# Kernel optimization log

Measured on AMD Instinct MI355X. Metric: run time of the kernel, lower is better.

Reference implementation:

```python
import jax, jax.numpy as jnp
import numpy as np

HIDDEN = 256
HEADS = 8
HEAD_DIM = HIDDEN // HEADS
SCALE = HEAD_DIM ** -0.5


def setup_inputs() -> dict:
    key = jax.random.key(0)
    ks = jax.random.split(key, 12)
    B, N = 2, 2048
    s = lambda fan_in: 1.0 / np.sqrt(fan_in)
    inp = {
        'x': jax.random.normal(ks[0], (B, N, HIDDEN), jnp.float32),
        'coords': jax.random.normal(ks[1], (B, N, 3), jnp.float32),
        'W_qkv': jax.random.normal(ks[2], (HIDDEN, 3 * HIDDEN), jnp.float32) * s(HIDDEN),
        'W_out': jax.random.normal(ks[3], (HIDDEN, HIDDEN), jnp.float32) * s(HIDDEN),
        'b_out': jnp.zeros((HIDDEN,), jnp.float32),
        'pos_w1': jax.random.normal(ks[4], (3, 16), jnp.float32) * s(3),
        'pos_b1': jnp.zeros((16,), jnp.float32),
        'pos_w2': jax.random.normal(ks[5], (16, HEADS), jnp.float32) * s(16),
        'pos_b2': jnp.zeros((HEADS,), jnp.float32),
        'sym_w1': jax.random.normal(ks[6], (3, 16), jnp.float32) * s(3),
        'sym_b1': jnp.zeros((16,), jnp.float32),
        'sym_w2': jax.random.normal(ks[7], (16, HEADS), jnp.float32) * s(16),
        'sym_b2': jnp.zeros((HEADS,), jnp.float32),
    }
    return inp


def _bias_mlp(rel, w1, b1, w2, b2):
    # rel: [B,N,N,3] -> [B,H,N,N]
    h = jax.nn.relu(jnp.einsum('bijc,ck->bijk', rel, w1) + b1)
    out = jnp.einsum('bijk,kh->bijh', h, w2) + b2
    return jnp.transpose(out, (0, 3, 1, 2))


def reference(x, coords, W_qkv, W_out, b_out, pos_w1, pos_b1, pos_w2, pos_b2,
              sym_w1, sym_b1, sym_w2, sym_b2):
    B, N, C = x.shape
    qkv = (x @ W_qkv).reshape(B, N, 3, HEADS, HEAD_DIM)
    qkv = jnp.transpose(qkv, (2, 0, 3, 1, 4))  # [3,B,H,N,D]
    q, k, v = qkv[0], qkv[1], qkv[2]
    dots = jnp.einsum('bhid,bhjd->bhij', q, k) * SCALE
    rel_pos = coords[:, :, None, :] - coords[:, None, :, :]  # [B,N,N,3]
    reflect = jnp.array([-1.0, 1.0, 1.0], dtype=coords.dtype)
    coords_sym = coords * reflect
    sym_rel_pos = coords[:, :, None, :] - coords_sym[:, None, :, :]
    bias_direct = _bias_mlp(rel_pos, pos_w1, pos_b1, pos_w2, pos_b2)
    bias_sym = _bias_mlp(sym_rel_pos, sym_w1, sym_b1, sym_w2, sym_b2)
    attn = jax.nn.softmax(dots + bias_direct + bias_sym, axis=-1)
    out = jnp.einsum('bhij,bhjd->bhid', attn, v)
    out = jnp.transpose(out, (0, 2, 1, 3)).reshape(B, N, C)
    return out @ W_out + b_out
```

## Files before the change

### kernel.cpp

```cpp
#include <hip/hip_runtime.h>
#include <hip/hip_fp16.h>

typedef _Float16 half8_t __attribute__((ext_vector_type(8)));
typedef _Float16 half4_t __attribute__((ext_vector_type(4)));
typedef _Float16 h2      __attribute__((ext_vector_type(2)));
typedef float    f32x4   __attribute__((ext_vector_type(4)));

#define LOG2E 1.4426950408889634f
#define KSCALE (0.17677669529663687f * LOG2E)

#if __has_builtin(__builtin_amdgcn_exp2f)
#define EXP2F(x) __builtin_amdgcn_exp2f(x)
#else
#define EXP2F(x) exp2f(x)
#endif

template <int N>
__device__ __forceinline__ int dpp_ror(int v) {
  return __builtin_amdgcn_update_dpp(0, v, 0x120 + N, 0xf, 0xf, true);
}
__device__ __forceinline__ h2 rowmax16_h2(h2 v) {
  int t;
  t = dpp_ror<1>(__builtin_bit_cast(int, v));
  v = __builtin_elementwise_max(v, __builtin_bit_cast(h2, t));
  t = dpp_ror<2>(__builtin_bit_cast(int, v));
  v = __builtin_elementwise_max(v, __builtin_bit_cast(h2, t));
  t = dpp_ror<4>(__builtin_bit_cast(int, v));
  v = __builtin_elementwise_max(v, __builtin_bit_cast(h2, t));
  t = dpp_ror<8>(__builtin_bit_cast(int, v));
  v = __builtin_elementwise_max(v, __builtin_bit_cast(h2, t));
  return v;
}

__global__ __launch_bounds__(256) void prep_misc(
    const float* __restrict__ Wqkv, const float* __restrict__ Wout,
    const float* __restrict__ coords,
    const float* __restrict__ pw1, const float* __restrict__ pb1,
    const float* __restrict__ sw1, const float* __restrict__ sb1,
    _Float16* __restrict__ WqkvT, _Float16* __restrict__ WoutT,
    _Float16* __restrict__ APre, _Float16* __restrict__ BPre)
{
  __shared__ float tile[64][65];
  const int bi = blockIdx.x, tid = threadIdx.x;
  if (bi < 64) {
    const float* src; _Float16* dst; int t, W;
    if (bi < 48) { t = bi;      src = Wqkv; dst = WqkvT; W = 768; }
    else         { t = bi - 48; src = Wout; dst = WoutT; W = 256; }
    const int nOT = W >> 6;
    const int tk = t / nOT, to = t % nOT;
    const int cx = tid & 63, ry = tid >> 6;
#pragma unroll
    for (int rr = 0; rr < 16; ++rr) {
      const int kl = rr * 4 + ry;
      tile[kl][cx] = src[(tk * 64 + kl) * W + to * 64 + cx];
    }
    __syncthreads();
#pragma unroll
    for (int rr = 0; rr < 16; ++rr) {
      const int ol = rr * 4 + ry;
      dst[(to * 64 + ol) * 256 + tk * 64 + cx] = (_Float16)tile[cx][ol];
    }
  } else {
    const int row = (bi - 64) * 256 + tid;
    const float c0 = coords[row * 3 + 0];
    const float c1 = coords[row * 3 + 1];
    const float c2 = coords[row * 3 + 2];
#pragma unroll
    for (int k = 0; k < 16; ++k) {
      float a = c0 * pw1[k] + c1 * pw1[16 + k] + c2 * pw1[32 + k];
      APre[row * 32 + k] = (_Float16)(a + pb1[k]);
      BPre[row * 32 + k] = (_Float16)a;
      float s  =  c0 * sw1[k] + c1 * sw1[16 + k] + c2 * sw1[32 + k];
      float sb = -c0 * sw1[k] + c1 * sw1[16 + k] + c2 * sw1[32 + k];
      APre[row * 32 + 16 + k] = (_Float16)(s + sb1[k]);
      BPre[row * 32 + 16 + k] = (_Float16)sb;
    }
  }
}

__global__ __launch_bounds__(256) void qkv_gemm(
    const float* __restrict__ x, const _Float16* __restrict__ WqkvT,
    _Float16* __restrict__ Qh, _Float16* __restrict__ Kh,
    _Float16* __restrict__ Vt)
{
  __shared__ __align__(16) _Float16 tbuf[4][1536];
  const int wv = threadIdx.x >> 6;
  const int wg = blockIdx.x * 4 + wv;
  const int ti = wg / 12, og = wg % 12;
  const int i0 = ti * 16, o0 = og * 64;
  const int lane = threadIdx.x & 63, q = lane >> 4, c = lane & 15;
  f32x4 acc[4] = {{0,0,0,0},{0,0,0,0},{0,0,0,0},{0,0,0,0}};
  const float*    arow = x + (i0 + c) * 256;
  const _Float16* brow = WqkvT + (o0 + c) * 256;
#pragma unroll
  for (int k0 = 0; k0 < 256; k0 += 32) {
    f32x4 a0 = *reinterpret_cast<const f32x4*>(arow + k0 + q * 8);
    f32x4 a1 = *reinterpret_cast<const f32x4*>(arow + k0 + q * 8 + 4);
    half8_t af;
    af[0] = (_Float16)a0[0]; af[1] = (_Float16)a0[1];
    af[2] = (_Float16)a0[2]; af[3] = (_Float16)a0[3];
    af[4] = (_Float16)a1[0]; af[5] = (_Float16)a1[1];
    af[6] = (_Float16)a1[2]; af[7] = (_Float16)a1[3];
#pragma unroll
    for (int t = 0; t < 4; ++t) {
      half8_t bf = *reinterpret_cast<const half8_t*>(brow + t * 16 * 256 + k0 + q * 8);
      acc[t] = __builtin_amdgcn_mfma_f32_16x16x32_f16(af, bf, acc[t], 0, 0, 0);
    }
  }
  const int b = i0 >> 11, n0 = i0 & 2047;
  _Float16* vt = tbuf[wv];
  if (og < 8) {
#pragma unroll
    for (int t = 0; t < 4; ++t)
#pragma unroll
      for (int r = 0; r < 4; ++r)
        vt[(q * 4 + r) * 72 + t * 16 + c] = (_Float16)acc[t][r];
    asm volatile("s_waitcnt lgkmcnt(0)" ::: "memory");
    __builtin_amdgcn_sched_barrier(0);
    const int nl = lane & 15, seg = lane >> 4;
    const int o_g = o0 + seg * 16;
    const int h = (o_g >> 5) & 7, dbase = o_g & 31;
    _Float16* dst = ((o_g >> 8) == 0 ? Qh : Kh) +
                    ((b * 8 + h) * 2048 + n0 + nl) * 32 + dbase;
    half8_t r0 = *reinterpret_cast<const half8_t*>(vt + nl * 72 + seg * 16);
    half8_t r1 = *reinterpret_cast<const half8_t*>(vt + nl * 72 + seg * 16 + 8);
    *reinterpret_cast<half8_t*>(dst)     = r0;
    *reinterpret_cast<half8_t*>(dst + 8) = r1;
  } else {
#pragma unroll
    for (int t = 0; t < 4; ++t)
#pragma unroll
      for (int r = 0; r < 4; ++r)
        vt[(t * 16 + c) * 24 + q * 4 + r] = (_Float16)acc[t][r];
    asm volatile("s_waitcnt lgkmcnt(0)" ::: "memory");
    __builtin_amdgcn_sched_barrier(0);
    const long row = (long)(b * 256 + (o0 - 512) + lane);
    half8_t r0 = *reinterpret_cast<const half8_t*>(vt + lane * 24);
    half8_t r1 = *reinterpret_cast<const half8_t*>(vt + lane * 24 + 8);
    *reinterpret_cast<half8_t*>(Vt + row * 2048 + n0)     = r0;
    *reinterpret_cast<half8_t*>(Vt + row * 2048 + n0 + 8) = r1;
  }
}

__global__ __launch_bounds__(512, 4) void flash(
    const _Float16* __restrict__ Qh, const _Float16* __restrict__ Kh,
    const _Float16* __restrict__ Vt, const _Float16* __restrict__ APre,
    const _Float16* __restrict__ BPre, const float* __restrict__ pw2,
    const float* __restrict__ sw2, _Float16* __restrict__ Opart,
    float* __restrict__ Mpart)
{
  __shared__ __align__(16) unsigned char smem[53504];
  _Float16* biasH = reinterpret_cast<_Float16*>(smem);
  _Float16* pbuf  = reinterpret_cast<_Float16*>(smem + 37120);

  const int blk = blockIdx.x;
  const int b     = blk >> 8;
  const int chunk = (blk >> 6) & 3;
  const int i0    = (blk & 63) << 5;
  const int tid = threadIdx.x;
  const int w = tid >> 6, lane = tid & 63;
  const int q = lane >> 4, c = lane & 15;

  const _Float16* qbase = Qh + ((b * 8 + w) * 2048 + i0) * 32;
  half8_t qfA = *reinterpret_cast<const half8_t*>(qbase + c * 32 + q * 8);
  half8_t qfB = *reinterpret_cast<const half8_t*>(qbase + (16 + c) * 32 + q * 8);
  const _Float16* abase = APre + (b * 2048 + i0) * 32;
  half8_t apfA = *reinterpret_cast<const half8_t*>(abase + c * 32 + q * 8);
  half8_t apfB = *reinterpret_cast<const half8_t*>(abase + (16 + c) * 32 + q * 8);

  half8_t w2f;
#pragma unroll
  for (int jj = 0; jj < 8; ++jj) {
    const int k = q * 8 + jj;
    float val = 0.f;
    if (c < 8) val = (k < 16 ? pw2[k * 8 + c] : sw2[(k - 16) * 8 + c]) * LOG2E;
    w2f[jj] = (_Float16)val;
  }
  half8_t ones8;
#pragma unroll
  for (int jj = 0; jj < 8; ++jj) ones8[jj] = (_Float16)1.0f;

  float mA[4], mB[4];
  f32x4 O0A = {0,0,0,0}, O1A = {0,0,0,0}, O0B = {0,0,0,0}, O1B = {0,0,0,0};
  f32x4 lpA = {0,0,0,0}, lpB = {0,0,0,0};
#pragma unroll
  for (int r = 0; r < 4; ++r) { mA[r] = 0.f; mB[r] = 0.f; }

  const f32x4 z4 = {0.f, 0.f, 0.f, 0.f};
  half8_t hzero8 = {};

  const int jbase = chunk * 512;
  const _Float16* BPre_b = BPre + (long)b * 2048 * 32;

  const int bwoff = c * 1160 + w * 144 + q * 4;
  const int broff = w * 1160 + c * 72 + q * 4;
  _Float16* pbA = pbuf + w * 1024;
  _Float16* pbB = pbA + 512;
  const int pwo = q * 128 + 2 * c;
  const int pro = c * 32 + q * 8;
  const _Float16* kb0 = Kh + ((b * 8 + w) * 2048 + jbase) * 32;
  const _Float16* vb0 = Vt + (b * 8 + w) * 65536 + jbase;
  const int ko0 = (2 * c) * 32 + q * 8, ko1 = ko0 + 32;
  const int vo0 = c * 2048 + q * 8,     vo1 = vo0 + 16 * 2048;
  const _Float16* bpb = BPre_b + (jbase + w * 4) * 32 + q * 8;

  half8_t pf0 = *reinterpret_cast<const half8_t*>(bpb);
  half8_t pf1 = *reinterpret_cast<const half8_t*>(bpb + 32);
  half8_t pf2 = *reinterpret_cast<const half8_t*>(bpb + 64);
  half8_t pf3 = *reinterpret_cast<const half8_t*>(bpb + 96);

  auto tile = [&](const int jt, _Float16* bH) {
    _Float16* bW = bH + bwoff;
#pragma unroll
    for (int mt = 0; mt < 4; ++mt) {
      half8_t bpf = (mt == 0) ? pf0 : (mt == 1) ? pf1 : (mt == 2) ? pf2 : pf3;
      half8_t hvA = __builtin_elementwise_max(apfA - bpf, hzero8);
      f32x4 bcA = __builtin_amdgcn_mfma_f32_16x16x32_f16(hvA, w2f, z4, 0, 0, 0);
      half8_t hvB = __builtin_elementwise_max(apfB - bpf, hzero8);
      f32x4 bcB = __builtin_amdgcn_mfma_f32_16x16x32_f16(hvB, w2f, z4, 0, 0, 0);
      if (c < 8) {
        half4_t b4;
        b4[0] = (_Float16)bcA[0]; b4[1] = (_Float16)bcA[1];
        b4[2] = (_Float16)bcA[2]; b4[3] = (_Float16)bcA[3];
        *reinterpret_cast<half4_t*>(bW + mt * 36) = b4;
        half4_t b5;
        b5[0] = (_Float16)bcB[0]; b5[1] = (_Float16)bcB[1];
        b5[2] = (_Float16)bcB[2]; b5[3] = (_Float16)bcB[3];
        *reinterpret_cast<half4_t*>(bW + mt * 36 + 16) = b5;
      }
    }

    const _Float16* kbase = kb0 + jt * 1024;
    const _Float16* vbase = vb0 + jt * 32;
    half8_t kf0 = *reinterpret_cast<const half8_t*>(kbase + ko0);
    half8_t kf1 = *reinterpret_cast<const half8_t*>(kbase + ko1);
    half8_t vf0 = *reinterpret_cast<const half8_t*>(vbase + vo0);
    half8_t vf1 = *reinterpret_cast<const half8_t*>(vbase + vo1);
    f32x4 sA0 = __builtin_amdgcn_mfma_f32_16x16x32_f16(qfA, kf0, z4, 0, 0, 0);
    f32x4 sA1 = __builtin_amdgcn_mfma_f32_16x16x32_f16(qfA, kf1, z4, 0, 0, 0);
    f32x4 sB0 = __builtin_amdgcn_mfma_f32_16x16x32_f16(qfB, kf0, z4, 0, 0, 0);
    f32x4 sB1 = __builtin_amdgcn_mfma_f32_16x16x32_f16(qfB, kf1, z4, 0, 0, 0);

    {
      const _Float16* bp = bpb + ((jt < 15) ? (jt + 1) : jt) * 1024;
      pf0 = *reinterpret_cast<const half8_t*>(bp);
      pf1 = *reinterpret_cast<const half8_t*>(bp + 32);
      pf2 = *reinterpret_cast<const half8_t*>(bp + 64);
      pf3 = *reinterpret_cast<const half8_t*>(bp + 96);
    }

    __syncthreads();

    const _Float16* bR = bH + broff;
    half4_t bbA0 = *reinterpret_cast<const half4_t*>(bR);
    half4_t bbA1 = *reinterpret_cast<const half4_t*>(bR + 36);
    half4_t bbB0 = *reinterpret_cast<const half4_t*>(bR + 16);
    half4_t bbB1 = *reinterpret_cast<const half4_t*>(bR + 52);

    {
      float svm0[4], svm1[4], p0[4], p1[4];
#pragma unroll
      for (int r = 0; r < 4; ++r) {
        const float bm0 = (float)bbA0[r] - mA[r];
        const float bm1 = (float)bbA1[r] - mA[r];
        svm0[r] = fmaf(sA0[r], KSCALE, bm0);
        svm1[r] = fmaf(sA1[r], KSCALE, bm1);
        p0[r] = EXP2F(svm0[r]);
        p1[r] = EXP2F(svm1[r]);
      }
      float need = fmaxf(fmaxf(fmaxf(svm0[0], svm1[0]), fmaxf(svm0[1], svm1[1])),
                         fmaxf(fmaxf(svm0[2], svm1[2]), fmaxf(svm0[3], svm1[3])));
      if (__any(need > 4.0f)) {
        float mr[4];
#pragma unroll
        for (int r = 0; r < 4; ++r) mr[r] = fmaxf(svm0[r], svm1[r]) + mA[r];
        h2 pk01, pk23;
        pk01[0] = (_Float16)mr[0]; pk01[1] = (_Float16)mr[1];
        pk23[0] = (_Float16)mr[2]; pk23[1] = (_Float16)mr[3];
        pk01 = rowmax16_h2(pk01);
        pk23 = rowmax16_h2(pk23);
        float mred[4] = {(float)pk01[0], (float)pk01[1],
                         (float)pk23[0], (float)pk23[1]};
#pragma unroll
        for (int r = 0; r < 4; ++r) {
          const float mnew = fmaxf(mA[r], mred[r]);
          const float alpha = EXP2F(mA[r] - mnew);
          p0[r] *= alpha; p1[r] *= alpha;
          lpA[r] *= alpha;
          O0A[r] *= alpha; O1A[r] *= alpha;
          mA[r] = mnew;
        }
      }
#pragma unroll
      for (int r = 0; r < 4; ++r) {
        h2 pp; pp[0] = (_Float16)p0[r]; pp[1] = (_Float16)p1[r];
        *reinterpret_cast<h2*>(pbA + pwo + r * 32) = pp;
      }
    }
    {
      float svm0[4], svm1[4], p0[4], p1[4];
#pragma unroll
      for (int r = 0; r < 4; ++r) {
        const float bm0 = (float)bbB0[r] - mB[r];
        const float bm1 = (float)bbB1[r] - mB[r];
        svm0[r] = fmaf(sB0[r], KSCALE, bm0);
        svm1[r] = fmaf(sB1[r], KSCALE, bm1);
        p0[r] = EXP2F(svm0[r]);
        p1[r] = EXP2F(svm1[r]);
      }
      float need = fmaxf(fmaxf(fmaxf(svm0[0], svm1[0]), fmaxf(svm0[1], svm1[1])),
                         fmaxf(fmaxf(svm0[2], svm1[2]), fmaxf(svm0[3], svm1[3])));
      if (__any(need > 4.0f)) {
        float mr[4];
#pragma unroll
        for (int r = 0; r < 4; ++r) mr[r] = fmaxf(svm0[r], svm1[r]) + mB[r];
        h2 pk01, pk23;
        pk01[0] = (_Float16)mr[0]; pk01[1] = (_Float16)mr[1];
        pk23[0] = (_Float16)mr[2]; pk23[1] = (_Float16)mr[3];
        pk01 = rowmax16_h2(pk01);
        pk23 = rowmax16_h2(pk23);
        float mred[4] = {(float)pk01[0], (float)pk01[1],
                         (float)pk23[0], (float)pk23[1]};
#pragma unroll
        for (int r = 0; r < 4; ++r) {
          const float mnew = fmaxf(mB[r], mred[r]);
          const float alpha = EXP2F(mB[r] - mnew);
          p0[r] *= alpha; p1[r] *= alpha;
          lpB[r] *= alpha;
          O0B[r] *= alpha; O1B[r] *= alpha;
          mB[r] = mnew;
        }
      }
#pragma unroll
      for (int r = 0; r < 4; ++r) {
        h2 pp; pp[0] = (_Float16)p0[r]; pp[1] = (_Float16)p1[r];
        *reinterpret_cast<h2*>(pbB + pwo + r * 32) = pp;
      }
    }

    asm volatile("s_waitcnt lgkmcnt(0)" ::: "memory");
    __builtin_amdgcn_sched_barrier(0);

    half8_t pfAx = *reinterpret_cast<const half8_t*>(pbA + pro);
    half8_t pfBx = *reinterpret_cast<const half8_t*>(pbB + pro);
    O0A = __builtin_amdgcn_mfma_f32_16x16x32_f16(pfAx, vf0, O0A, 0, 0, 0);
    O1A = __builtin_amdgcn_mfma_f32_16x16x32_f16(pfAx, vf1, O1A, 0, 0, 0);
    O0B = __builtin_amdgcn_mfma_f32_16x16x32_f16(pfBx, vf0, O0B, 0, 0, 0);
    O1B = __builtin_amdgcn_mfma_f32_16x16x32_f16(pfBx, vf1, O1B, 0, 0, 0);
    lpA = __builtin_amdgcn_mfma_f32_16x16x32_f16(pfAx, ones8, lpA, 0, 0, 0);
    lpB = __builtin_amdgcn_mfma_f32_16x16x32_f16(pfBx, ones8, lpB, 0, 0, 0);
  };

  for (int pt = 0; pt < 8; ++pt) {
    tile(2 * pt,     biasH);
    tile(2 * pt + 1, biasH + 9280);
  }

#pragma unroll
  for (int r = 0; r < 4; ++r) {
    const float s = lpA[r];
    const float inv = 1.f / s;
    const int n = i0 + q * 4 + r;
    const long base = (long)(((chunk * 2 + b) * 8 + w) * 2048 + n);
    Opart[base * 32 + c]      = (_Float16)(O0A[r] * inv);
    Opart[base * 32 + 16 + c] = (_Float16)(O1A[r] * inv);
    if (c == 0) Mpart[base] = mA[r] + __log2f(s);
  }
#pragma unroll
  for (int r = 0; r < 4; ++r) {
    const float s = lpB[r];
    const float inv = 1.f / s;
    const int n = i0 + 16 + q * 4 + r;
    const long base = (long)(((chunk * 2 + b) * 8 + w) * 2048 + n);
    Opart[base * 32 + c]      = (_Float16)(O0B[r] * inv);
    Opart[base * 32 + 16 + c] = (_Float16)(O1B[r] * inv);
    if (c == 0) Mpart[base] = mB[r] + __log2f(s);
  }
}

__global__ __launch_bounds__(256) void combine_proj(
    const _Float16* __restrict__ Opart, const float* __restrict__ Mpart,
    const _Float16* __restrict__ WoutT, const float* __restrict__ bout,
    float* __restrict__ out)
{
  __shared__ _Float16 aT[16][264];
  const int i0 = blockIdx.x * 16;
  const int b = i0 >> 11;
  const int n0 = i0 & 2047;
  const int tid = threadIdx.x;
  {
    const int row = tid >> 4, cg = tid & 15;
    const int n = n0 + row;
    const int h = cg >> 1;
    const int d0 = (cg & 1) * 16;
    float mv[4], M = -INFINITY;
#pragma unroll
    for (int ck = 0; ck < 4; ++ck) {
      mv[ck] = Mpart[((ck * 2 + b) * 8 + h) * 2048 + n];
      M = fmaxf(M, mv[ck]);
    }
    float num[16];
#pragma unroll
    for (int e = 0; e < 16; ++e) num[e] = 0.f;
    float den = 0.f;
#pragma unroll
    for (int ck = 0; ck < 4; ++ck) {
      const float wgt = EXP2F(mv[ck] - M);
      const _Float16* op = Opart +
          (long)(((ck * 2 + b) * 8 + h) * 2048 + n) * 32 + d0;
      half8_t o0v = *reinterpret_cast<const half8_t*>(op);
      half8_t o1v = *reinterpret_cast<const half8_t*>(op + 8);
#pragma unroll
      for (int e = 0; e < 8; ++e) {
        num[e]     += wgt * (float)o0v[e];
        num[8 + e] += wgt * (float)o1v[e];
      }
      den += wgt;
    }
    const float inv = 1.f / den;
    half8_t h0, h1;
#pragma unroll
    for (int e = 0; e < 8; ++e) {
      h0[e] = (_Float16)(num[e] * inv);
      h1[e] = (_Float16)(num[8 + e] * inv);
    }
    *reinterpret_cast<half8_t*>(&aT[row][cg * 16])     = h0;
    *reinterpret_cast<half8_t*>(&aT[row][cg * 16 + 8]) = h1;
  }
  __syncthreads();

  const int o0 = (tid >> 6) * 64;
  const int lane = tid & 63, q = lane >> 4, c = lane & 15;
  f32x4 acc[4] = {{0,0,0,0},{0,0,0,0},{0,0,0,0},{0,0,0,0}};
  const _Float16* brow = WoutT + (o0 + c) * 256;
#pragma unroll
  for (int k0 = 0; k0 < 256; k0 += 32) {
    half8_t af = *reinterpret_cast<const half8_t*>(&aT[c][k0 + q * 8]);
#pragma unroll
    for (int t = 0; t < 4; ++t) {
      half8_t bf = *reinterpret_cast<const half8_t*>(brow + t * 16 * 256 + k0 + q * 8);
      acc[t] = __builtin_amdgcn_mfma_f32_16x16x32_f16(af, bf, acc[t], 0, 0, 0);
    }
  }
#pragma unroll
  for (int t = 0; t < 4; ++t) {
    const float bo = bout[o0 + t * 16 + c];
#pragma unroll
    for (int r = 0; r < 4; ++r)
      out[(i0 + q * 4 + r) * 256 + o0 + t * 16 + c] = acc[t][r] + bo;
  }
}

extern "C" void kernel_launch(void* const* d_in, const int* in_sizes, int n_in,
                              void* d_out, int out_size, void* d_ws, size_t ws_size,
                              hipStream_t stream)
{
  const float* x      = (const float*)d_in[0];
  const float* coords = (const float*)d_in[1];
  const float* Wqkv   = (const float*)d_in[2];
  const float* Wout   = (const float*)d_in[3];
  const float* bout   = (const float*)d_in[4];
  const float* pw1    = (const float*)d_in[5];
  const float* pb1    = (const float*)d_in[6];
  const float* pw2    = (const float*)d_in[7];
  const float* sw1    = (const float*)d_in[9];
  const float* sb1    = (const float*)d_in[10];
  const float* sw2    = (const float*)d_in[11];
  float* out = (float*)d_out;

  char* ws = (char*)d_ws;
  _Float16* Qh      = (_Float16*)(ws + 0);
  _Float16* Kh      = (_Float16*)(ws + 2097152);
  _Float16* Vt      = (_Float16*)(ws + 4194304);
  _Float16* WqkvT   = (_Float16*)(ws + 8388608);
  _Float16* WoutT   = (_Float16*)(ws + 8781824);
  _Float16* APre    = (_Float16*)(ws + 8912896);
  _Float16* BPre    = (_Float16*)(ws + 9175040);
  _Float16* Opart   = (_Float16*)(ws + 9437184);
  float*    Mpart   = (float*)   (ws + 17825792);

  prep_misc<<<80, 256, 0, stream>>>(Wqkv, Wout, coords, pw1, pb1, sw1, sb1,
                                    WqkvT, WoutT, APre, BPre);
  qkv_gemm<<<768, 256, 0, stream>>>(x, WqkvT, Qh, Kh, Vt);
  flash<<<512, 512, 0, stream>>>(Qh, Kh, Vt, APre, BPre, pw2, sw2, Opart, Mpart);
  combine_proj<<<256, 256, 0, stream>>>(Opart, Mpart, WoutT, bout, out);
}
```

Before: 157.6 us.

## Software-pipeline bias MLP production one tile ahead with double-buffered LDS

Bias tiles for the next key tile are now computed into the alternate LDS buffer while the current tile's bias is read, with a prologue that fills the first buffer before the loop. The barrier moves to the end of each tile, so the bias-production MFMAs and LDS writes can overlap with the QK, softmax and PV work instead of sitting in front of a barrier every tile. Prefetch of the bias MLP inputs now runs two tiles ahead. The cost is more live registers and a different placement of synchronisation, which could lower occupancy or add a hazard if the buffer indexing is wrong.

```diff
diff --git a/kernel.cpp b/kernel.cpp
--- a/kernel.cpp
+++ b/kernel.cpp
@@ -204,16 +204,12 @@
   const int vo0 = c * 2048 + q * 8,     vo1 = vo0 + 16 * 2048;
   const _Float16* bpb = BPre_b + (jbase + w * 4) * 32 + q * 8;
 
-  half8_t pf0 = *reinterpret_cast<const half8_t*>(bpb);
-  half8_t pf1 = *reinterpret_cast<const half8_t*>(bpb + 32);
-  half8_t pf2 = *reinterpret_cast<const half8_t*>(bpb + 64);
-  half8_t pf3 = *reinterpret_cast<const half8_t*>(bpb + 96);
-
-  auto tile = [&](const int jt, _Float16* bH) {
+  auto bias_prod = [&](_Float16* bH, half8_t f0, half8_t f1, half8_t f2,
+                       half8_t f3) {
     _Float16* bW = bH + bwoff;
 #pragma unroll
     for (int mt = 0; mt < 4; ++mt) {
-      half8_t bpf = (mt == 0) ? pf0 : (mt == 1) ? pf1 : (mt == 2) ? pf2 : pf3;
+      half8_t bpf = (mt == 0) ? f0 : (mt == 1) ? f1 : (mt == 2) ? f2 : f3;
       half8_t hvA = __builtin_elementwise_max(apfA - bpf, hzero8);
       f32x4 bcA = __builtin_amdgcn_mfma_f32_16x16x32_f16(hvA, w2f, z4, 0, 0, 0);
       half8_t hvB = __builtin_elementwise_max(apfB - bpf, hzero8);
@@ -229,6 +225,39 @@
         *reinterpret_cast<half4_t*>(bW + mt * 36 + 16) = b5;
       }
     }
+  };
+
+  {
+    half8_t t0 = *reinterpret_cast<const half8_t*>(bpb);
+    half8_t t1 = *reinterpret_cast<const half8_t*>(bpb + 32);
+    half8_t t2 = *reinterpret_cast<const half8_t*>(bpb + 64);
+    half8_t t3 = *reinterpret_cast<const half8_t*>(bpb + 96);
+    bias_prod(biasH, t0, t1, t2, t3);
+  }
+  half8_t pf0 = *reinterpret_cast<const half8_t*>(bpb + 1024);
+  half8_t pf1 = *reinterpret_cast<const half8_t*>(bpb + 1024 + 32);
+  half8_t pf2 = *reinterpret_cast<const half8_t*>(bpb + 1024 + 64);
+  half8_t pf3 = *reinterpret_cast<const half8_t*>(bpb + 1024 + 96);
+  __syncthreads();
+
+  auto tile = [&](const int jt, _Float16* bufR, _Float16* bufW,
+                  const bool last) {
+    const _Float16* bR = bufR + broff;
+    half4_t bbA0 = *reinterpret_cast<const half4_t*>(bR);
+    half4_t bbA1 = *reinterpret_cast<const half4_t*>(bR + 36);
+    half4_t bbB0 = *reinterpret_cast<const half4_t*>(bR + 16);
+    half4_t bbB1 = *reinterpret_cast<const half4_t*>(bR + 52);
+
+    if (!last) bias_prod(bufW, pf0, pf1, pf2, pf3);
+
+    {
+      const int jn = (jt + 2 < 16) ? (jt + 2) : 15;
+      const _Float16* bp = bpb + jn * 1024;
+      pf0 = *reinterpret_cast<const half8_t*>(bp);
+      pf1 = *reinterpret_cast<const half8_t*>(bp + 32);
+      pf2 = *reinterpret_cast<const half8_t*>(bp + 64);
+      pf3 = *reinterpret_cast<const half8_t*>(bp + 96);
+    }
 
     const _Float16* kbase = kb0 + jt * 1024;
     const _Float16* vbase = vb0 + jt * 32;
@@ -242,22 +271,6 @@
     f32x4 sB1 = __builtin_amdgcn_mfma_f32_16x16x32_f16(qfB, kf1, z4, 0, 0, 0);
 
     {
-      const _Float16* bp = bpb + ((jt < 15) ? (jt + 1) : jt) * 1024;
-      pf0 = *reinterpret_cast<const half8_t*>(bp);
-      pf1 = *reinterpret_cast<const half8_t*>(bp + 32);
-      pf2 = *reinterpret_cast<const half8_t*>(bp + 64);
-      pf3 = *reinterpret_cast<const half8_t*>(bp + 96);
-    }
-
-    __syncthreads();
-
-    const _Float16* bR = bH + broff;
-    half4_t bbA0 = *reinterpret_cast<const half4_t*>(bR);
-    half4_t bbA1 = *reinterpret_cast<const half4_t*>(bR + 36);
-    half4_t bbB0 = *reinterpret_cast<const half4_t*>(bR + 16);
-    half4_t bbB1 = *reinterpret_cast<const half4_t*>(bR + 52);
-
-    {
       float svm0[4], svm1[4], p0[4], p1[4];
 #pragma unroll
       for (int r = 0; r < 4; ++r) {
@@ -349,11 +362,13 @@
     O1B = __builtin_amdgcn_mfma_f32_16x16x32_f16(pfBx, vf1, O1B, 0, 0, 0);
     lpA = __builtin_amdgcn_mfma_f32_16x16x32_f16(pfAx, ones8, lpA, 0, 0, 0);
     lpB = __builtin_amdgcn_mfma_f32_16x16x32_f16(pfBx, ones8, lpB, 0, 0, 0);
+
+    if (!last) __syncthreads();
   };
 
   for (int pt = 0; pt < 8; ++pt) {
-    tile(2 * pt,     biasH);
-    tile(2 * pt + 1, biasH + 9280);
+    tile(2 * pt,     biasH,        biasH + 9280, false);
+    tile(2 * pt + 1, biasH + 9280, biasH,        pt == 7);
   }
 
 #pragma unroll
```

Measured after the change: 163.6 us. 1.04x slower.
